# Optimization experiments

Hardware: AMD Instinct MI355X
Metric: run time of the kernel (lower is better)

Reference implementation:

```python
import jax, jax.numpy as jnp
import numpy as np

N = 1024   # nodes
C = 256    # channels (n_features)
NEG_SLOPE = 0.2


def setup_inputs() -> dict:
    key = jax.random.key(0)
    k1, k2, k3, k4, k5, k6, k7 = jax.random.split(key, 7)
    nodes = jax.random.normal(k1, (N, C), dtype=jnp.float32)
    # dense adjacency used only via (adj != 0); force self-loops so every
    # softmax row has at least one valid entry
    adj_mat = jax.random.randint(k2, (N, N), 0, 2).astype(jnp.int32)
    adj_mat = adj_mat.at[jnp.arange(N), jnp.arange(N)].set(1)
    lim = 1.0 / np.sqrt(C)  # eqx.nn.Linear default uniform init bound
    W_src_w = jax.random.uniform(k3, (C, C), minval=-lim, maxval=lim, dtype=jnp.float32)
    W_src_b = jax.random.uniform(k4, (C,), minval=-lim, maxval=lim, dtype=jnp.float32)
    W_tgt_w = jax.random.uniform(k5, (C, C), minval=-lim, maxval=lim, dtype=jnp.float32)
    W_tgt_b = jax.random.uniform(k6, (C,), minval=-lim, maxval=lim, dtype=jnp.float32)
    a_w = jax.random.uniform(k7, (C,), minval=-lim, maxval=lim, dtype=jnp.float32)  # to_score, no bias
    return {"nodes": nodes, "adj_mat": adj_mat, "W_src_w": W_src_w, "W_src_b": W_src_b,
            "W_tgt_w": W_tgt_w, "W_tgt_b": W_tgt_b, "a_w": a_w}


def reference(nodes, adj_mat, W_src_w, W_src_b, W_tgt_w, W_tgt_b, a_w):
    # per-node linear maps (eqx.nn.Linear: y = W @ x + b)
    g_src = nodes @ W_src_w.T + W_src_b              # [node, C]
    g_tgt = nodes @ W_tgt_w.T + W_tgt_b              # [node, C]
    # g[i, j, c] = g_src[i, c] + g_tgt[j, c]   (axis names as in original: tgt, src)
    g = g_src[:, None, :] + g_tgt[None, :, :]        # [node, node, C]
    g = jax.nn.leaky_relu(g, NEG_SLOPE)
    score = jnp.einsum('ijc,c->ij', g, a_w)          # [node, node]
    score = jnp.where(adj_mat != 0, score, -jnp.inf) # mask non-edges
    weights = jax.nn.softmax(score, axis=1)          # over src axis
    return weights @ g_tgt                           # [node, C]
```

## Files before the change

kernel.cpp:

```cpp
#include <hip/hip_runtime.h>


typedef unsigned short u16;
typedef unsigned int   u32;
typedef _Float16 h2 __attribute__((ext_vector_type(2)));

#define NNODE 1024
#define NC    256
#define NEG   0.2f

__device__ __forceinline__ float bf2f(u16 h) {
    u32 u = ((u32)h) << 16;
    return __builtin_bit_cast(float, u);
}
__device__ __forceinline__ u16 f2bf(float f) {
    u32 u = __builtin_bit_cast(u32, f);
    u32 r = (u + 0x7FFFu + ((u >> 16) & 1u)) >> 16;
    return (u16)r;
}
__device__ __forceinline__ u16 f2h(float f) {
    _Float16 h = (_Float16)f;
    return __builtin_bit_cast(u16, h);
}
__device__ __forceinline__ h2 bch(u32 u) { return __builtin_bit_cast(h2, u); }

__device__ __forceinline__ h2 lrelu2(h2 y) {
    h2 yn = y * (_Float16)NEG;
#if __has_builtin(__builtin_elementwise_max)
    return __builtin_elementwise_max(y, yn);
#else
    h2 r; r.x = y.x > yn.x ? y.x : yn.x; r.y = y.y > yn.y ? y.y : yn.y;
    return r;
#endif
}
__device__ __forceinline__ float dot2(h2 a, h2 b, float acc) {
#if __has_builtin(__builtin_amdgcn_fdot2)
    return __builtin_amdgcn_fdot2(a, b, acc, false);
#else
    acc = fmaf((float)a.x, (float)b.x, acc);
    return fmaf((float)a.y, (float)b.y, acc);
#endif
}

__device__ __forceinline__ int wave_detect(const u16* __restrict__ nodes, int lane)
{
    ushort4 v = *(const ushort4*)(nodes + lane * 4);
    const u16 h[4] = {v.x, v.y, v.z, v.w};
    int cnt = 0;
    #pragma unroll
    for (int q = 0; q < 4; ++q) {
        int e = (h[q] >> 7) & 0xFF;
        cnt += (e >= 132 || (e >= 1 && e <= 90)) ? 1 : 0;
    }
    #pragma unroll
    for (int off = 32; off; off >>= 1) cnt += __shfl_xor(cnt, off, 64);
    return (cnt >= 64) ? 0 : 1;
}

__device__ __forceinline__ int swz(int grp, int row) { return grp ^ (row & 31); }

__global__ __launch_bounds__(256) void lin_kernel(
    const void* __restrict__ nodes_v,
    const void* __restrict__ Wsrc_v, const void* __restrict__ bsrc_v,
    const void* __restrict__ Wtgt_v, const void* __restrict__ btgt_v,
    u16* __restrict__ gsh, u16* __restrict__ gth)
{
    __shared__ float nT[64][34];
    __shared__ float wT[64][68];

    const int t  = threadIdx.x;
    const int bf = wave_detect((const u16*)nodes_v, t & 63);
    const int ct = blockIdx.x;
    const int it = blockIdx.y;
    const int i0 = it * 32;
    const bool is_src = (ct < 4);
    const int c0 = (is_src ? ct : ct - 4) * 64;
    const void* __restrict__ Wv = is_src ? Wsrc_v : Wtgt_v;
    const void* __restrict__ bv = is_src ? bsrc_v : btgt_v;
    u16* __restrict__ g         = is_src ? gsh : gth;

    const int tc = t & 15, ti = t >> 4;
    float acc[2][4] = {};

    for (int k0 = 0; k0 < NC; k0 += 64) {
        __syncthreads();
        {
            int ii = t & 31, kg = t >> 5;
            float vals[8];
            if (bf) {
                uint4 v = *(const uint4*)((const u16*)nodes_v + (i0 + ii) * NC + k0 + kg * 8);
                const u16* pv = (const u16*)&v;
                #pragma unroll
                for (int q = 0; q < 8; ++q) vals[q] = bf2f(pv[q]);
            } else {
                const float* nf = (const float*)nodes_v;
                float4 v0 = *(const float4*)(nf + (i0 + ii) * NC + k0 + kg * 8);
                float4 v1 = *(const float4*)(nf + (i0 + ii) * NC + k0 + kg * 8 + 4);
                vals[0] = v0.x; vals[1] = v0.y; vals[2] = v0.z; vals[3] = v0.w;
                vals[4] = v1.x; vals[5] = v1.y; vals[6] = v1.z; vals[7] = v1.w;
            }
            #pragma unroll
            for (int q = 0; q < 8; ++q) nT[kg * 8 + q][ii] = vals[q];
        }
        {
            int cc = t & 63, kg = t >> 6;
            float vals[16];
            if (bf) {
                const u16* W = (const u16*)Wv;
                uint4 v0 = *(const uint4*)(W + (c0 + cc) * NC + k0 + kg * 16);
                uint4 v1 = *(const uint4*)(W + (c0 + cc) * NC + k0 + kg * 16 + 8);
                const u16* p0 = (const u16*)&v0;
                const u16* p1 = (const u16*)&v1;
                #pragma unroll
                for (int q = 0; q < 8; ++q) { vals[q] = bf2f(p0[q]); vals[8 + q] = bf2f(p1[q]); }
            } else {
                const float* W = (const float*)Wv;
                #pragma unroll
                for (int h = 0; h < 4; ++h) {
                    float4 v = *(const float4*)(W + (c0 + cc) * NC + k0 + kg * 16 + 4 * h);
                    vals[4 * h + 0] = v.x; vals[4 * h + 1] = v.y;
                    vals[4 * h + 2] = v.z; vals[4 * h + 3] = v.w;
                }
            }
            #pragma unroll
            for (int q = 0; q < 16; ++q) wT[kg * 16 + q][cc] = vals[q];
        }
        __syncthreads();
        #pragma unroll 8
        for (int kk = 0; kk < 64; ++kk) {
            float2 av = *(const float2*)&nT[kk][2 * ti];
            float4 bvv = *(const float4*)&wT[kk][4 * tc];
            float sa[2] = {av.x, av.y};
            float tb[4] = {bvv.x, bvv.y, bvv.z, bvv.w};
            #pragma unroll
            for (int a = 0; a < 2; ++a)
                #pragma unroll
                for (int b = 0; b < 4; ++b)
                    acc[a][b] = fmaf(sa[a], tb[b], acc[a][b]);
        }
    }

    float bb[4];
    #pragma unroll
    for (int q = 0; q < 4; ++q)
        bb[q] = bf ? bf2f(((const u16*)bv)[c0 + 4 * tc + q])
                   : ((const float*)bv)[c0 + 4 * tc + q];
    #pragma unroll
    for (int a = 0; a < 2; ++a) {
        int irow = i0 + 2 * ti + a;
        ushort4 ov;
        ov.x = f2h(acc[a][0] + bb[0]);
        ov.y = f2h(acc[a][1] + bb[1]);
        ov.z = f2h(acc[a][2] + bb[2]);
        ov.w = f2h(acc[a][3] + bb[3]);
        *(ushort4*)(g + (size_t)irow * NC + c0 + 4 * tc) = ov;
    }
}

__global__ __launch_bounds__(256, 4) void fused_kernel(
    const u16* __restrict__ gsh, const u16* __restrict__ gth,
    const void* __restrict__ aw_v, const int* __restrict__ adj,
    const u16* __restrict__ nodes_u16, int jcnt,
    float* __restrict__ po, float* __restrict__ pm,
    float* __restrict__ pls, void* __restrict__ out_v)
{
    __shared__ u32   gt32[64 * 128];
    __shared__ u32   a32[128];
    __shared__ float p_lds[8][64];

    const int t    = threadIdx.x;
    const int wv   = t >> 6;
    const int lane = t & 63;
    const int bf   = wave_detect(nodes_u16, lane);
    const int r0   = blockIdx.x * 8 + 2 * wv;
    const int z    = blockIdx.y;
    const int jbase = z * jcnt;
    const int jl = lane & 15, q  = lane >> 4;
    const int oc = lane & 31, hh = lane >> 5;

    if (t < 128) {
        float a0, a1;
        if (bf) { a0 = bf2f(((const u16*)aw_v)[2 * t]); a1 = bf2f(((const u16*)aw_v)[2 * t + 1]); }
        else    { a0 = ((const float*)aw_v)[2 * t];     a1 = ((const float*)aw_v)[2 * t + 1]; }
        h2 av; av.x = (_Float16)a0; av.y = (_Float16)a1;
        a32[t] = __builtin_bit_cast(u32, av);
    }

    u32 gsr[2][32];
    #pragma unroll
    for (int r = 0; r < 2; ++r) {
        const u16* src = gsh + (size_t)(r0 + r) * NC + q * 64;
        #pragma unroll
        for (int k = 0; k < 8; ++k) {
            uint4 gv = *(const uint4*)(src + 8 * k);
            gsr[r][4 * k + 0] = gv.x; gsr[r][4 * k + 1] = gv.y;
            gsr[r][4 * k + 2] = gv.z; gsr[r][4 * k + 3] = gv.w;
        }
    }

    float m[2] = {-1e30f, -1e30f}, l[2] = {0.f, 0.f};
    float of[2][8] = {};

    for (int j0 = jbase; j0 < jbase + jcnt; j0 += 64) {
        __syncthreads();
        {
            int rr = t & 63, seg = t >> 6;
            const u16* src = gth + (size_t)(j0 + rr) * NC + seg * 64;
            u32* dst = gt32 + rr * 128;
            #pragma unroll
            for (int k = 0; k < 8; ++k) {
                uint4 v = *(const uint4*)(src + 8 * k);
                *(uint4*)(dst + swz(seg * 8 + k, rr) * 4) = v;
            }
        }
        __syncthreads();

        float spv[2][4] = {};
        #pragma unroll
        for (int k = 0; k < 8; ++k) {
            uint4 a4 = *(const uint4*)&a32[q * 32 + 4 * k];
            h2 a0 = bch(a4.x), a1 = bch(a4.y), a2 = bch(a4.z), a3 = bch(a4.w);
            #pragma unroll
            for (int p = 0; p < 4; ++p) {
                const int rowp = 16 * p + jl;
                uint4 g4 = *(const uint4*)&gt32[rowp * 128 + swz(q * 8 + k, rowp) * 4];
                h2 t0 = bch(g4.x), t1 = bch(g4.y), t2 = bch(g4.z), t3 = bch(g4.w);
                #pragma unroll
                for (int r = 0; r < 2; ++r) {
                    spv[r][p] = dot2(a0, lrelu2(bch(gsr[r][4 * k + 0]) + t0), spv[r][p]);
                    spv[r][p] = dot2(a1, lrelu2(bch(gsr[r][4 * k + 1]) + t1), spv[r][p]);
                    spv[r][p] = dot2(a2, lrelu2(bch(gsr[r][4 * k + 2]) + t2), spv[r][p]);
                    spv[r][p] = dot2(a3, lrelu2(bch(gsr[r][4 * k + 3]) + t3), spv[r][p]);
                }
            }
        }
        #pragma unroll
        for (int r = 0; r < 2; ++r)
            #pragma unroll
            for (int p = 0; p < 4; ++p) {
                spv[r][p] += __shfl_xor(spv[r][p], 16, 64);
                spv[r][p] += __shfl_xor(spv[r][p], 32, 64);
            }

        float alpha[2];
        #pragma unroll
        for (int r = 0; r < 2; ++r) {
            const float s = (lane < 16) ? spv[r][0] : (lane < 32) ? spv[r][1]
                          : (lane < 48) ? spv[r][2] : spv[r][3];
            const int valid = adj[(size_t)(r0 + r) * NNODE + j0 + lane];
            float sm = valid ? s : -1e30f;
            float tmax = sm;
            #pragma unroll
            for (int off = 32; off; off >>= 1)
                tmax = fmaxf(tmax, __shfl_xor(tmax, off, 64));
            const float mn = fmaxf(m[r], tmax);
            alpha[r]       = __expf(m[r] - mn);
            const float p  = valid ? __expf(s - mn) : 0.f;
            float ps = p;
            #pragma unroll
            for (int off = 32; off; off >>= 1) ps += __shfl_xor(ps, off, 64);
            l[r] = l[r] * alpha[r] + ps;
            m[r] = mn;
            p_lds[2 * wv + r][lane] = p;
        }

        #pragma unroll
        for (int r = 0; r < 2; ++r)
            #pragma unroll
            for (int k = 0; k < 8; ++k) of[r][k] *= alpha[r];

        #pragma unroll 4
        for (int jp = 0; jp < 32; ++jp) {
            const int j = 2 * jp + hh;
            const float w0 = p_lds[2 * wv    ][j];
            const float w1 = p_lds[2 * wv + 1][j];
            uint4 g4 = *(const uint4*)&gt32[j * 128 + swz(oc, j) * 4];
            h2 v0 = bch(g4.x), v1 = bch(g4.y), v2 = bch(g4.z), v3 = bch(g4.w);
            of[0][0] = fmaf(w0, (float)v0.x, of[0][0]);
            of[0][1] = fmaf(w0, (float)v0.y, of[0][1]);
            of[0][2] = fmaf(w0, (float)v1.x, of[0][2]);
            of[0][3] = fmaf(w0, (float)v1.y, of[0][3]);
            of[0][4] = fmaf(w0, (float)v2.x, of[0][4]);
            of[0][5] = fmaf(w0, (float)v2.y, of[0][5]);
            of[0][6] = fmaf(w0, (float)v3.x, of[0][6]);
            of[0][7] = fmaf(w0, (float)v3.y, of[0][7]);
            of[1][0] = fmaf(w1, (float)v0.x, of[1][0]);
            of[1][1] = fmaf(w1, (float)v0.y, of[1][1]);
            of[1][2] = fmaf(w1, (float)v1.x, of[1][2]);
            of[1][3] = fmaf(w1, (float)v1.y, of[1][3]);
            of[1][4] = fmaf(w1, (float)v2.x, of[1][4]);
            of[1][5] = fmaf(w1, (float)v2.y, of[1][5]);
            of[1][6] = fmaf(w1, (float)v3.x, of[1][6]);
            of[1][7] = fmaf(w1, (float)v3.y, of[1][7]);
        }
    }

    #pragma unroll
    for (int r = 0; r < 2; ++r)
        #pragma unroll
        for (int k = 0; k < 8; ++k) of[r][k] += __shfl_xor(of[r][k], 32, 64);

    if (lane < 32) {
        #pragma unroll
        for (int r = 0; r < 2; ++r) {
            const int row = r0 + r;
            if (out_v) {
                const float inv = 1.0f / l[r];
                if (bf) {
                    u16* out = (u16*)out_v;
                    ushort4 oa, ob;
                    oa.x = f2bf(of[r][0] * inv); oa.y = f2bf(of[r][1] * inv);
                    oa.z = f2bf(of[r][2] * inv); oa.w = f2bf(of[r][3] * inv);
                    ob.x = f2bf(of[r][4] * inv); ob.y = f2bf(of[r][5] * inv);
                    ob.z = f2bf(of[r][6] * inv); ob.w = f2bf(of[r][7] * inv);
                    *(ushort4*)(out + (size_t)row * NC + 8 * oc)     = oa;
                    *(ushort4*)(out + (size_t)row * NC + 8 * oc + 4) = ob;
                } else {
                    float* out = (float*)out_v;
                    *(float4*)(out + (size_t)row * NC + 8 * oc) =
                        make_float4(of[r][0] * inv, of[r][1] * inv,
                                    of[r][2] * inv, of[r][3] * inv);
                    *(float4*)(out + (size_t)row * NC + 8 * oc + 4) =
                        make_float4(of[r][4] * inv, of[r][5] * inv,
                                    of[r][6] * inv, of[r][7] * inv);
                }
            } else {
                float* pp = po + ((size_t)z * NNODE + row) * NC + 8 * oc;
                *(float4*)pp       = make_float4(of[r][0], of[r][1], of[r][2], of[r][3]);
                *(float4*)(pp + 4) = make_float4(of[r][4], of[r][5], of[r][6], of[r][7]);
            }
        }
    }
    if (!out_v && lane == 0) {
        #pragma unroll
        for (int r = 0; r < 2; ++r) {
            pm [(size_t)z * NNODE + r0 + r] = m[r];
            pls[(size_t)z * NNODE + r0 + r] = l[r];
        }
    }
}

__global__ __launch_bounds__(256) void combine_kernel(
    const float* __restrict__ po, const float* __restrict__ pm,
    const float* __restrict__ pls, const u16* __restrict__ nodes_u16,
    int ns, void* __restrict__ out_v)
{
    const int bf  = wave_detect(nodes_u16, threadIdx.x & 63);
    const int row = blockIdx.x;
    const int c   = threadIdx.x;

    float mstar = -1e30f;
    for (int zz = 0; zz < ns; ++zz)
        mstar = fmaxf(mstar, pm[zz * NNODE + row]);

    float acc = 0.f, lsum = 0.f;
    for (int zz = 0; zz < ns; ++zz) {
        const float wz = __expf(pm[zz * NNODE + row] - mstar);
        lsum = fmaf(pls[zz * NNODE + row], wz, lsum);
        acc  = fmaf(po[(size_t)(zz * NNODE + row) * NC + c], wz, acc);
    }
    const float v = acc / lsum;
    if (bf) ((u16*)out_v)[row * NC + c] = f2bf(v);
    else    ((float*)out_v)[row * NC + c] = v;
}

extern "C" void kernel_launch(void* const* d_in, const int* in_sizes, int n_in,
                              void* d_out, int out_size, void* d_ws, size_t ws_size,
                              hipStream_t stream)
{
    const u16* nodes_u16 = (const u16*)d_in[0];
    const int* adj       = (const int*)d_in[1];

    char* wsb = (char*)d_ws;
    u16* gsh  = (u16*)wsb;
    u16* gth  = gsh + (size_t)NNODE * NC;

    lin_kernel<<<dim3(8, 32), 256, 0, stream>>>(d_in[0], d_in[2], d_in[3],
                                                d_in[4], d_in[5], gsh, gth);

    const size_t base = 2ull * NNODE * NC * sizeof(u16);
    const size_t per  = 4ull * NNODE * NC + 8ull * NNODE;
    int NS = 0;
    if      (ws_size >= base + 8 * per) NS = 8;
    else if (ws_size >= base + 4 * per) NS = 4;
    else if (ws_size >= base + 2 * per) NS = 2;

    if (NS) {
        float* po  = (float*)(wsb + base);
        float* pm  = po + (size_t)NS * NNODE * NC;
        float* pls = pm + (size_t)NS * NNODE;
        fused_kernel<<<dim3(128, NS), 256, 0, stream>>>(
            gsh, gth, d_in[6], adj, nodes_u16, NNODE / NS, po, pm, pls, nullptr);
        combine_kernel<<<NNODE, 256, 0, stream>>>(po, pm, pls, nodes_u16, NS, d_out);
    } else {
        fused_kernel<<<dim3(128, 1), 256, 0, stream>>>(
            gsh, gth, d_in[6], adj, nodes_u16, NNODE, nullptr, nullptr, nullptr, d_out);
    }
}
```

Baseline: 72.13 us.

## Rewrite leaky ReLU as linear plus abs term, enlarge fused blocks

Uses the identity leaky_relu(x) = 0.6x + 0.4|x| so the inner score loop only computes a dot of the scaled weights with |gs+gt|. The linear parts become per-row and per-column scalar terms. The per-target term is precomputed by a new small kernel, and the per-source term is computed once per row at block start. This replaces the fp16 multiply+max in the hot loop with a bitmask abs. The fused kernel also grows to 512 threads and 16 rows per block, so each shared tile of g_tgt is reused across more rows, at the cost of an extra launch and lower occupancy hints.

After: 64.58 us. -10.5%, faster.

```diff
diff --git a/kernel.cpp b/kernel.cpp
--- a/kernel.cpp
+++ b/kernel.cpp
@@ -23,15 +23,9 @@
     return __builtin_bit_cast(u16, h);
 }
 __device__ __forceinline__ h2 bch(u32 u) { return __builtin_bit_cast(h2, u); }
-
-__device__ __forceinline__ h2 lrelu2(h2 y) {
-    h2 yn = y * (_Float16)NEG;
-#if __has_builtin(__builtin_elementwise_max)
-    return __builtin_elementwise_max(y, yn);
-#else
-    h2 r; r.x = y.x > yn.x ? y.x : yn.x; r.y = y.y > yn.y ? y.y : yn.y;
-    return r;
-#endif
+__device__ __forceinline__ h2 habs2(h2 y) {
+    u32 u = __builtin_bit_cast(u32, y) & 0x7FFF7FFFu;
+    return __builtin_bit_cast(h2, u);
 }
 __device__ __forceinline__ float dot2(h2 a, h2 b, float acc) {
 #if __has_builtin(__builtin_amdgcn_fdot2)
@@ -157,22 +151,49 @@
     }
 }
 
-__global__ __launch_bounds__(256, 4) void fused_kernel(
+__global__ __launch_bounds__(256) void sdot_kernel(
+    const u16* __restrict__ gth, const void* __restrict__ aw_v,
+    const u16* __restrict__ nodes_u16, float* __restrict__ sgt06)
+{
+    const int t    = threadIdx.x;
+    const int lane = t & 63;
+    const int bf   = wave_detect(nodes_u16, lane);
+    const int row  = blockIdx.x * 4 + (t >> 6);
+
+    float a0, a1, a2, a3;
+    if (bf) {
+        ushort4 a4 = *(const ushort4*)((const u16*)aw_v + lane * 4);
+        a0 = bf2f(a4.x); a1 = bf2f(a4.y); a2 = bf2f(a4.z); a3 = bf2f(a4.w);
+    } else {
+        float4 a4 = *(const float4*)((const float*)aw_v + lane * 4);
+        a0 = a4.x; a1 = a4.y; a2 = a4.z; a3 = a4.w;
+    }
+    ushort4 gv = *(const ushort4*)(gth + (size_t)row * NC + lane * 4);
+    float s = a0 * (float)__builtin_bit_cast(_Float16, gv.x)
+            + a1 * (float)__builtin_bit_cast(_Float16, gv.y)
+            + a2 * (float)__builtin_bit_cast(_Float16, gv.z)
+            + a3 * (float)__builtin_bit_cast(_Float16, gv.w);
+    #pragma unroll
+    for (int off = 32; off; off >>= 1) s += __shfl_xor(s, off, 64);
+    if (lane == 0) sgt06[row] = 0.6f * s;
+}
+
+__global__ __launch_bounds__(512, 2) void fused_kernel(
     const u16* __restrict__ gsh, const u16* __restrict__ gth,
     const void* __restrict__ aw_v, const int* __restrict__ adj,
-    const u16* __restrict__ nodes_u16, int jcnt,
-    float* __restrict__ po, float* __restrict__ pm,
+    const u16* __restrict__ nodes_u16, const float* __restrict__ sgt06,
+    int jcnt, float* __restrict__ po, float* __restrict__ pm,
     float* __restrict__ pls, void* __restrict__ out_v)
 {
     __shared__ u32   gt32[64 * 128];
     __shared__ u32   a32[128];
-    __shared__ float p_lds[8][64];
+    __shared__ float p_lds[16][64];
 
     const int t    = threadIdx.x;
-    const int wv   = t >> 6;
+    const int i    = t >> 6;
     const int lane = t & 63;
     const int bf   = wave_detect(nodes_u16, lane);
-    const int r0   = blockIdx.x * 8 + 2 * wv;
+    const int r0   = blockIdx.x * 16 + 2 * i;
     const int z    = blockIdx.y;
     const int jbase = z * jcnt;
     const int jl = lane & 15, q  = lane >> 4;
@@ -182,7 +203,7 @@
         float a0, a1;
         if (bf) { a0 = bf2f(((const u16*)aw_v)[2 * t]); a1 = bf2f(((const u16*)aw_v)[2 * t + 1]); }
         else    { a0 = ((const float*)aw_v)[2 * t];     a1 = ((const float*)aw_v)[2 * t + 1]; }
-        h2 av; av.x = (_Float16)a0; av.y = (_Float16)a1;
+        h2 av; av.x = (_Float16)(0.4f * a0); av.y = (_Float16)(0.4f * a1);
         a32[t] = __builtin_bit_cast(u32, av);
     }
 
@@ -197,6 +218,24 @@
             gsr[r][4 * k + 2] = gv.z; gsr[r][4 * k + 3] = gv.w;
         }
     }
+    __syncthreads();
+
+    float Sgs06[2];
+    #pragma unroll
+    for (int r = 0; r < 2; ++r) {
+        float sg = 0.f;
+        #pragma unroll
+        for (int k = 0; k < 8; ++k) {
+            uint4 a4 = *(const uint4*)&a32[q * 32 + 4 * k];
+            sg = dot2(bch(a4.x), bch(gsr[r][4 * k + 0]), sg);
+            sg = dot2(bch(a4.y), bch(gsr[r][4 * k + 1]), sg);
+            sg = dot2(bch(a4.z), bch(gsr[r][4 * k + 2]), sg);
+            sg = dot2(bch(a4.w), bch(gsr[r][4 * k + 3]), sg);
+        }
+        sg += __shfl_xor(sg, 16, 64);
+        sg += __shfl_xor(sg, 32, 64);
+        Sgs06[r] = 1.5f * sg;
+    }
 
     float m[2] = {-1e30f, -1e30f}, l[2] = {0.f, 0.f};
     float of[2][8] = {};
@@ -204,16 +243,18 @@
     for (int j0 = jbase; j0 < jbase + jcnt; j0 += 64) {
         __syncthreads();
         {
-            int rr = t & 63, seg = t >> 6;
-            const u16* src = gth + (size_t)(j0 + rr) * NC + seg * 64;
+            int rr = t & 63, kg = t >> 6;
+            const u16* src = gth + (size_t)(j0 + rr) * NC + kg * 32;
             u32* dst = gt32 + rr * 128;
             #pragma unroll
-            for (int k = 0; k < 8; ++k) {
-                uint4 v = *(const uint4*)(src + 8 * k);
-                *(uint4*)(dst + swz(seg * 8 + k, rr) * 4) = v;
+            for (int c = 0; c < 4; ++c) {
+                uint4 v = *(const uint4*)(src + 8 * c);
+                *(uint4*)(dst + swz(kg * 4 + c, rr) * 4) = v;
             }
         }
         __syncthreads();
+
+        const float sgtj = sgt06[j0 + lane];
 
         float spv[2][4] = {};
         #pragma unroll
@@ -227,10 +268,10 @@
                 h2 t0 = bch(g4.x), t1 = bch(g4.y), t2 = bch(g4.z), t3 = bch(g4.w);
                 #pragma unroll
                 for (int r = 0; r < 2; ++r) {
-                    spv[r][p] = dot2(a0, lrelu2(bch(gsr[r][4 * k + 0]) + t0), spv[r][p]);
-                    spv[r][p] = dot2(a1, lrelu2(bch(gsr[r][4 * k + 1]) + t1), spv[r][p]);
-                    spv[r][p] = dot2(a2, lrelu2(bch(gsr[r][4 * k + 2]) + t2), spv[r][p]);
-                    spv[r][p] = dot2(a3, lrelu2(bch(gsr[r][4 * k + 3]) + t3), spv[r][p]);
+                    spv[r][p] = dot2(a0, habs2(bch(gsr[r][4 * k + 0]) + t0), spv[r][p]);
+                    spv[r][p] = dot2(a1, habs2(bch(gsr[r][4 * k + 1]) + t1), spv[r][p]);
+                    spv[r][p] = dot2(a2, habs2(bch(gsr[r][4 * k + 2]) + t2), spv[r][p]);
+                    spv[r][p] = dot2(a3, habs2(bch(gsr[r][4 * k + 3]) + t3), spv[r][p]);
                 }
             }
         }
@@ -245,8 +286,9 @@
         float alpha[2];
         #pragma unroll
         for (int r = 0; r < 2; ++r) {
-            const float s = (lane < 16) ? spv[r][0] : (lane < 32) ? spv[r][1]
-                          : (lane < 48) ? spv[r][2] : spv[r][3];
+            const float sabs = (lane < 16) ? spv[r][0] : (lane < 32) ? spv[r][1]
+                             : (lane < 48) ? spv[r][2] : spv[r][3];
+            const float s = sabs + Sgs06[r] + sgtj;
             const int valid = adj[(size_t)(r0 + r) * NNODE + j0 + lane];
             float sm = valid ? s : -1e30f;
             float tmax = sm;
@@ -261,19 +303,18 @@
             for (int off = 32; off; off >>= 1) ps += __shfl_xor(ps, off, 64);
             l[r] = l[r] * alpha[r] + ps;
             m[r] = mn;
-            p_lds[2 * wv + r][lane] = p;
+            p_lds[2 * i + r][lane] = p;
         }
 
         #pragma unroll
         for (int r = 0; r < 2; ++r)
             #pragma unroll
             for (int k = 0; k < 8; ++k) of[r][k] *= alpha[r];
-
         #pragma unroll 4
         for (int jp = 0; jp < 32; ++jp) {
             const int j = 2 * jp + hh;
-            const float w0 = p_lds[2 * wv    ][j];
-            const float w1 = p_lds[2 * wv + 1][j];
+            const float w0 = p_lds[2 * i    ][j];
+            const float w1 = p_lds[2 * i + 1][j];
             uint4 g4 = *(const uint4*)&gt32[j * 128 + swz(oc, j) * 4];
             h2 v0 = bch(g4.x), v1 = bch(g4.y), v2 = bch(g4.z), v3 = bch(g4.w);
             of[0][0] = fmaf(w0, (float)v0.x, of[0][0]);
@@ -371,14 +412,16 @@
     const u16* nodes_u16 = (const u16*)d_in[0];
     const int* adj       = (const int*)d_in[1];
 
-    char* wsb = (char*)d_ws;
-    u16* gsh  = (u16*)wsb;
-    u16* gth  = gsh + (size_t)NNODE * NC;
+    char*  wsb   = (char*)d_ws;
+    u16*   gsh   = (u16*)wsb;
+    u16*   gth   = gsh + (size_t)NNODE * NC;
+    float* sgt06 = (float*)(wsb + 2ull * NNODE * NC * sizeof(u16));
 
     lin_kernel<<<dim3(8, 32), 256, 0, stream>>>(d_in[0], d_in[2], d_in[3],
                                                 d_in[4], d_in[5], gsh, gth);
-
-    const size_t base = 2ull * NNODE * NC * sizeof(u16);
+    sdot_kernel<<<256, 256, 0, stream>>>(gth, d_in[6], nodes_u16, sgt06);
+
+    const size_t base = 2ull * NNODE * NC * sizeof(u16) + NNODE * sizeof(float);
     const size_t per  = 4ull * NNODE * NC + 8ull * NNODE;
     int NS = 0;
     if      (ws_size >= base + 8 * per) NS = 8;
@@ -389,11 +432,13 @@
         float* po  = (float*)(wsb + base);
         float* pm  = po + (size_t)NS * NNODE * NC;
         float* pls = pm + (size_t)NS * NNODE;
-        fused_kernel<<<dim3(128, NS), 256, 0, stream>>>(
-            gsh, gth, d_in[6], adj, nodes_u16, NNODE / NS, po, pm, pls, nullptr);
+        fused_kernel<<<dim3(64, NS), 512, 0, stream>>>(
+            gsh, gth, d_in[6], adj, nodes_u16, sgt06, NNODE / NS,
+            po, pm, pls, nullptr);
         combine_kernel<<<NNODE, 256, 0, stream>>>(po, pm, pls, nodes_u16, NS, d_out);
     } else {
-        fused_kernel<<<dim3(128, 1), 256, 0, stream>>>(
-            gsh, gth, d_in[6], adj, nodes_u16, NNODE, nullptr, nullptr, nullptr, d_out);
-    }
-}
+        fused_kernel<<<dim3(64, 1), 512, 0, stream>>>(
+            gsh, gth, d_in[6], adj, nodes_u16, sgt06, NNODE,
+            nullptr, nullptr, nullptr, d_out);
+    }
+}
```
